# Kernel optimization log

Hardware: AMD Instinct MI355X
Metric: run time of the kernel (lower is better)

Reference implementation:

```python
import jax, jax.numpy as jnp
import numpy as np

FP8_MAX = 448.0  # float8_e4m3fn max
NUM_HEADS = 16

def _fp8_quant_dequant(t):
    # per-(batch, head) symmetric scaling into fp8 e4m3 range, cast to fp8 and back
    amax = jnp.max(jnp.abs(t), axis=(-2, -1), keepdims=True)
    scale = FP8_MAX / jnp.maximum(amax, 1e-12)
    t8 = (t * scale).astype(jnp.float8_e4m3fn).astype(t.dtype)
    return t8 / scale

def setup_inputs() -> dict:
    key = jax.random.key(0)
    k1, k2, k3 = jax.random.split(key, 3)
    B, N, C = 2, 2048, 1024
    x = jax.random.normal(k1, (B, N, C), dtype=jnp.float32)
    w_qkv = jax.random.normal(k2, (C, 3 * C), dtype=jnp.float32) * (C ** -0.5)
    w_proj = jax.random.normal(k3, (C, C), dtype=jnp.float32) * (C ** -0.5)
    b_proj = jnp.zeros((C,), dtype=jnp.float32)
    return {"x": x, "w_qkv": w_qkv, "w_proj": w_proj, "b_proj": b_proj}

def reference(x, w_qkv, w_proj, b_proj):
    B, N, C = x.shape
    H = NUM_HEADS
    D = C // H
    scale = D ** -0.5
    qkv = (x @ w_qkv).reshape(B, N, 3, H, D).transpose(2, 0, 3, 1, 4)  # [3,B,H,N,D]
    q, k, v = qkv[0], qkv[1], qkv[2]
    # sage-style fp8 quantize/dequant of q and k fused into score computation
    q = _fp8_quant_dequant(q)
    k = _fp8_quant_dequant(k)
    scores = jnp.einsum('bhqd,bhkd->bhqk', q, k) * scale  # [B,H,N,N]
    causal = jnp.tril(jnp.ones((N, N), dtype=bool))
    scores = jnp.where(causal[None, None], scores, jnp.finfo(scores.dtype).min)
    attn = jax.nn.softmax(scores, axis=-1)
    out = jnp.einsum('bhqk,bhkd->bhqd', attn, v)  # [B,H,N,D]
    out = out.transpose(0, 2, 1, 3).reshape(B, N, C)
    return out @ w_proj + b_proj
```

## Files before the change

kernel.cpp:

```cpp
#include <hip/hip_runtime.h>

#define B_   2
#define N_   2048
#define C_   1024
#define H_   16
#define D_   64
#define BH_  (B_*H_)
#define NDH  (N_*D_)
#define M1   (B_*N_)

typedef __attribute__((ext_vector_type(4))) float    f32x4;
typedef __attribute__((ext_vector_type(8))) _Float16 f16x8;
typedef __attribute__((ext_vector_type(4))) _Float16 f16x4;
typedef __attribute__((ext_vector_type(2))) __fp16   h16x2;

#define GLOAD_LDS(gp, lp) \
  __builtin_amdgcn_global_load_lds((const __attribute__((address_space(1))) void*)(gp), \
                                   (__attribute__((address_space(3))) void*)(lp), 16, 0, 0)

__global__ __launch_bounds__(256) void k_prep(const float* __restrict__ x,
                                              _Float16* __restrict__ xh,
                                              const float* __restrict__ wq,
                                              const float* __restrict__ wp,
                                              _Float16* __restrict__ whT,
                                              _Float16* __restrict__ wpT,
                                              unsigned* __restrict__ amax_u) {
  __shared__ _Float16 t[64][68];
  int bid = blockIdx.x;
  if (bid < 4096) {
    int i = bid * 256 + threadIdx.x;
    float4 v = ((const float4*)x)[i];
    f16x4 o;
    o.x = (_Float16)v.x; o.y = (_Float16)v.y; o.z = (_Float16)v.z; o.w = (_Float16)v.w;
    ((f16x4*)xh)[i] = o;
    return;
  }
  int idx = bid - 4096;
  if (idx == 0 && threadIdx.x < 64) amax_u[threadIdx.x] = 0u;
  const float* in; _Float16* out; int Cc, cx, cy;
  if (idx < 768) { in = wq; out = whT; Cc = 3072; cx = idx % 48; cy = idx / 48; }
  else { idx -= 768; in = wp; out = wpT; Cc = 1024; cx = idx % 16; cy = idx / 16; }
  const int R = 1024;
  int c0 = cx * 64, r0 = cy * 64;
  int tid = threadIdx.x;
  int cq = tid & 15, rq = tid >> 4;
#pragma unroll
  for (int i = 0; i < 4; ++i) {
    int r = rq + i * 16;
    float4 v = *(const float4*)(in + (size_t)(r0 + r) * Cc + c0 + cq * 4);
    t[r][cq*4+0] = (_Float16)v.x;
    t[r][cq*4+1] = (_Float16)v.y;
    t[r][cq*4+2] = (_Float16)v.z;
    t[r][cq*4+3] = (_Float16)v.w;
  }
  __syncthreads();
#pragma unroll
  for (int i = 0; i < 4; ++i) {
    int c = rq + i * 16;
    f16x4 o;
    o.x = t[cq*4+0][c];
    o.y = t[cq*4+1][c];
    o.z = t[cq*4+2][c];
    o.w = t[cq*4+3][c];
    *(f16x4*)(out + (size_t)(c0 + c) * R + r0 + cq * 4) = o;
  }
}

__global__ __launch_bounds__(256) void k_gemm_qkv(const _Float16* __restrict__ A,
                                                  const _Float16* __restrict__ BT,
                                                  _Float16* __restrict__ qh,
                                                  _Float16* __restrict__ kh,
                                                  _Float16* __restrict__ vh,
                                                  unsigned* __restrict__ amax_u) {
  __shared__ __align__(16) _Float16 As[2][128 * 64];
  __shared__ __align__(16) _Float16 Bs[2][128 * 64];
  const int tid = threadIdx.x, lane = tid & 63, wave = tid >> 6;
  const int wm = wave >> 1, wn = wave & 1;
  const int mcol = lane & 15, quad = lane >> 4;
  const int m0 = blockIdx.x * 128, n0 = blockIdx.y * 128;
  const int swa = mcol & 7;
  f32x4 acc[4][4] = {};

  auto stage = [&](int buf, int k0) {
#pragma unroll
    for (int r = 0; r < 4; ++r) {
      int s = tid + r * 256;
      int row = s >> 3, kc = (s & 7) ^ (row & 7);
      GLOAD_LDS(A  + (size_t)(m0 + row) * 1024 + k0 + kc * 8, &As[buf][s * 8]);
      GLOAD_LDS(BT + (size_t)(n0 + row) * 1024 + k0 + kc * 8, &Bs[buf][s * 8]);
    }
  };
  auto compute = [&](int buf) {
#pragma unroll
    for (int kk = 0; kk < 2; ++kk) {
      f16x8 af[4], bf[4];
#pragma unroll
      for (int tm = 0; tm < 4; ++tm) {
        int row = wm * 64 + tm * 16 + mcol;
        af[tm] = *(const f16x8*)&As[buf][(row * 8 + ((kk * 4 + quad) ^ swa)) * 8];
      }
#pragma unroll
      for (int tn = 0; tn < 4; ++tn) {
        int row = wn * 64 + tn * 16 + mcol;
        bf[tn] = *(const f16x8*)&Bs[buf][(row * 8 + ((kk * 4 + quad) ^ swa)) * 8];
      }
#pragma unroll
      for (int tm = 0; tm < 4; ++tm)
#pragma unroll
        for (int tn = 0; tn < 4; ++tn)
          acc[tm][tn] = __builtin_amdgcn_mfma_f32_16x16x32_f16(af[tm], bf[tn], acc[tm][tn], 0, 0, 0);
    }
  };

  stage(0, 0);
#pragma unroll 1
  for (int t = 0; t < 16; ++t) {
    const int cur = t & 1;
    __builtin_amdgcn_s_barrier();
    if (t + 1 < 16) {
      stage(cur ^ 1, (t + 1) * 64);
      asm volatile("s_waitcnt vmcnt(8)" ::: "memory");
    } else {
      asm volatile("s_waitcnt vmcnt(0)" ::: "memory");
    }
    __builtin_amdgcn_s_barrier();
    __builtin_amdgcn_sched_barrier(0);
    compute(cur);
  }

  const int sec = n0 >> 10;
  if (sec < 2) {
    _Float16* dst = sec ? kh : qh;
    float mxv = 0.f;
#pragma unroll
    for (int tm = 0; tm < 4; ++tm)
#pragma unroll
      for (int tn = 0; tn < 4; ++tn) {
        int rowb = m0 + wm * 64 + tm * 16 + quad * 4;
        int col = n0 + wn * 64 + tn * 16 + mcol;
        int cc = col & 1023, h = cc >> 6, d = cc & 63;
        int b = rowb >> 11, n = rowb & 2047;
        f32x4 a = acc[tm][tn];
        mxv = fmaxf(mxv, fmaxf(fmaxf(fabsf(a[0]), fabsf(a[1])),
                               fmaxf(fabsf(a[2]), fabsf(a[3]))));
        f16x4 o;
        o.x = (_Float16)a[0]; o.y = (_Float16)a[1];
        o.z = (_Float16)a[2]; o.w = (_Float16)a[3];
        *(f16x4*)&dst[(size_t)(b * 16 + h) * 131072 + (size_t)(n >> 5) * 2048 + d * 32 + (n & 31)] = o;
      }
#pragma unroll
    for (int off = 32; off; off >>= 1) mxv = fmaxf(mxv, __shfl_xor(mxv, off));
    if (lane == 0) {
      int head = ((n0 & 1023) >> 6) + wn;
      int plane = (m0 >> 11) * 16 + head;
      atomicMax(&amax_u[sec * 32 + plane], __float_as_uint(mxv));
    }
  } else {
#pragma unroll
    for (int tm = 0; tm < 4; ++tm)
#pragma unroll
      for (int tn = 0; tn < 4; ++tn) {
        int rowb = m0 + wm * 64 + tm * 16 + quad * 4;
        int col = n0 + wn * 64 + tn * 16 + mcol;
        int cc = col & 1023, h = cc >> 6, d = cc & 63;
        int b = rowb >> 11, n = rowb & 2047;
        f16x4 o;
        o.x = (_Float16)acc[tm][tn][0];
        o.y = (_Float16)acc[tm][tn][1];
        o.z = (_Float16)acc[tm][tn][2];
        o.w = (_Float16)acc[tm][tn][3];
        size_t e = (size_t)(b * 16 + h) * 131072 + (size_t)(n >> 5) * 2048
                 + (d >> 4) * 512 + ((n >> 3) & 3) * 128 + (d & 15) * 8 + (n & 7);
        *(f16x4*)&vh[e] = o;
      }
  }
}

__global__ __launch_bounds__(256) void k_quant(const _Float16* __restrict__ qh,
                                               const _Float16* __restrict__ kh,
                                               const float* __restrict__ amax,
                                               char* __restrict__ q8,
                                               char* __restrict__ k8) {
  __shared__ ushort T[32][72];
  int blk = blockIdx.x;
  int which = blk >> 11;
  int idx = blk & 2047;
  int bh = idx >> 6, chunk = idx & 63;
  const _Float16* src = (which ? kh : qh) + (size_t)bh * NDH + chunk * 2048;
  float s = 448.f / fmaxf(amax[which * 32 + bh], 1e-12f);
  int t = threadIdx.x;
  f16x8 v = *(const f16x8*)(src + t * 8);
  int d = t >> 2, kk0 = (t & 3) * 8;
#pragma unroll
  for (int j = 0; j < 8; ++j) T[kk0 + j][d] = ((const ushort*)&v)[j];
  __syncthreads();
  int r = t >> 3, d0 = (t & 7) * 8;
  f16x8 row = *(const f16x8*)&T[r][d0];
  float f[8];
#pragma unroll
  for (int j = 0; j < 8; ++j) f[j] = (float)((const _Float16*)&row)[j] * s;
  int lo = 0, hi = 0;
  lo = __builtin_amdgcn_cvt_pk_fp8_f32(f[0], f[1], lo, false);
  lo = __builtin_amdgcn_cvt_pk_fp8_f32(f[2], f[3], lo, true);
  hi = __builtin_amdgcn_cvt_pk_fp8_f32(f[4], f[5], hi, false);
  hi = __builtin_amdgcn_cvt_pk_fp8_f32(f[6], f[7], hi, true);
  int2 o; o.x = lo; o.y = hi;
  if (which == 0) {
    char* dst = q8 + (size_t)bh * NDH + (size_t)(chunk * 32 + r) * 64 + d0;
    *(int2*)dst = o;
  } else {
    int e = (r >> 2) & 1;
    int mc = (r >> 3) * 4 + (r & 3);
    int kb = d0 >> 5, dq = (d0 >> 3) & 3;
    char* dst = k8 + (size_t)bh * NDH + chunk * 2048 + (e * 2 + kb) * 512 + dq * 128 + mc * 8;
    *(int2*)dst = o;
  }
}

__global__ __launch_bounds__(256) void k_flash(const char* __restrict__ q8,
                                               const char* __restrict__ k8,
                                               const _Float16* __restrict__ vh,
                                               const float* __restrict__ amax,
                                               _Float16* __restrict__ attn) {
  const int bh = blockIdx.x;
  const int tid = threadIdx.x;
  const int wave = tid >> 6, lane = tid & 63;
  const int mcol = lane & 15, quad = lane >> 4;
  const int g = 127 - (blockIdx.y * 4 + wave);
  const int nt = (g >> 3) + 1;
  const int ntmax = ((127 - blockIdx.y * 4) >> 3) + 1;

  __shared__ __align__(16) char     Ks[8192];
  __shared__ __align__(16) _Float16 Vs[8192];

  float sq = 448.f / fmaxf(amax[bh], 1e-12f);
  float sk = 448.f / fmaxf(amax[32 + bh], 1e-12f);
  const float c2 = (1.f / (sq * sk)) * 0.125f * 1.44269504089f;

  const size_t pbase = (size_t)bh * NDH;
  const char* kpl = k8 + pbase;
  const _Float16* vpl = vh + pbase;
  const int qrow = g * 16 + mcol;
  long aq0, aq1;
  { const char* qp = q8 + pbase + (size_t)qrow * 64;
    aq0 = *(const long*)(qp + quad * 8); aq1 = *(const long*)(qp + 32 + quad * 8); }

  f32x4 O[4] = {};
  float m_i = -3e38f, l_i = 0.f;
  const int b = bh >> 4, h = bh & 15;
  const int kq = quad * 8;
  const int koff = quad * 128 + mcol * 8;
  const int voff = quad * 128 + mcol * 8;

#pragma unroll 1
  for (int t = 0; t < ntmax; ++t) {
    {
      const char* ks = kpl + (size_t)t * 8192;
      const _Float16* vs = vpl + (size_t)t * 8192;
#pragma unroll
      for (int r = 0; r < 2; ++r)
        GLOAD_LDS(ks + (tid + r * 256) * 16, &Ks[(tid + r * 256) * 16]);
#pragma unroll
      for (int r = 0; r < 4; ++r)
        GLOAD_LDS(vs + (tid + r * 256) * 8, &Vs[(tid + r * 256) * 8]);
    }
    __syncthreads();

    if (t < nt) {
      const int n0 = t * 128;
      f32x4 s[4][2];
#pragma unroll
      for (int p = 0; p < 4; ++p)
#pragma unroll
        for (int e = 0; e < 2; ++e) {
          long ka = *(const long*)&Ks[(p * 4 + e * 2 + 0) * 512 + koff];
          long kb = *(const long*)&Ks[(p * 4 + e * 2 + 1) * 512 + koff];
          f32x4 z = {};
          z = __builtin_amdgcn_mfma_f32_16x16x32_fp8_fp8(ka, aq0, z, 0, 0, 0);
          z = __builtin_amdgcn_mfma_f32_16x16x32_fp8_fp8(kb, aq1, z, 0, 0, 0);
          s[p][e] = z;
        }
      if (t >= nt - 1) {
#pragma unroll
        for (int p = 0; p < 4; ++p)
#pragma unroll
          for (int e = 0; e < 2; ++e)
#pragma unroll
            for (int r = 0; r < 4; ++r) {
              int key = n0 + p * 32 + kq + e * 4 + r;
              s[p][e][r] = (key <= qrow) ? s[p][e][r] : -3e38f;
            }
      }
      float fm[8];
#pragma unroll
      for (int p = 0; p < 4; ++p)
#pragma unroll
        for (int e = 0; e < 2; ++e) {
          f32x4 v = s[p][e];
          fm[p * 2 + e] = fmaxf(fmaxf(v[0], v[1]), fmaxf(v[2], v[3]));
        }
      float mx = fmaxf(fmaxf(fmaxf(fm[0], fm[1]), fmaxf(fm[2], fm[3])),
                       fmaxf(fmaxf(fm[4], fm[5]), fmaxf(fm[6], fm[7])));
      mx = fmaxf(mx, m_i);
      mx = fmaxf(mx, __shfl_xor(mx, 16));
      mx = fmaxf(mx, __shfl_xor(mx, 32));
      float alpha = __builtin_amdgcn_exp2f((m_i - mx) * c2);
      m_i = mx;
      const float nh = -mx * c2;
      float fs[8];
#pragma unroll
      for (int p = 0; p < 4; ++p)
#pragma unroll
        for (int e = 0; e < 2; ++e) {
          float p0 = __builtin_amdgcn_exp2f(fmaf(s[p][e][0], c2, nh));
          float p1 = __builtin_amdgcn_exp2f(fmaf(s[p][e][1], c2, nh));
          float p2 = __builtin_amdgcn_exp2f(fmaf(s[p][e][2], c2, nh));
          float p3 = __builtin_amdgcn_exp2f(fmaf(s[p][e][3], c2, nh));
          s[p][e][0] = p0; s[p][e][1] = p1; s[p][e][2] = p2; s[p][e][3] = p3;
          fs[p * 2 + e] = (p0 + p1) + (p2 + p3);
        }
      float sum = ((fs[0] + fs[1]) + (fs[2] + fs[3])) + ((fs[4] + fs[5]) + (fs[6] + fs[7]));
      sum += __shfl_xor(sum, 16);
      sum += __shfl_xor(sum, 32);
      l_i = l_i * alpha + sum;
#pragma unroll
      for (int dt = 0; dt < 4; ++dt)
#pragma unroll
        for (int r = 0; r < 4; ++r)
          O[dt][r] *= alpha;
#pragma unroll
      for (int p = 0; p < 4; ++p) {
        f16x8 pb;
        h16x2* pb2 = (h16x2*)&pb;
        pb2[0] = __builtin_amdgcn_cvt_pkrtz(s[p][0][0], s[p][0][1]);
        pb2[1] = __builtin_amdgcn_cvt_pkrtz(s[p][0][2], s[p][0][3]);
        pb2[2] = __builtin_amdgcn_cvt_pkrtz(s[p][1][0], s[p][1][1]);
        pb2[3] = __builtin_amdgcn_cvt_pkrtz(s[p][1][2], s[p][1][3]);
#pragma unroll
        for (int dt = 0; dt < 4; ++dt) {
          f16x8 va = *(const f16x8*)&Vs[p * 2048 + dt * 512 + voff];
          O[dt] = __builtin_amdgcn_mfma_f32_16x16x32_f16(va, pb, O[dt], 0, 0, 0);
        }
      }
    }
    __syncthreads();
  }

  float rl = __builtin_amdgcn_rcpf(l_i);
  _Float16* op = attn + ((size_t)b * 2048 + qrow) * 1024 + h * 64;
#pragma unroll
  for (int dt = 0; dt < 4; ++dt) {
    f16x4 o;
    o.x = (_Float16)(O[dt][0] * rl);
    o.y = (_Float16)(O[dt][1] * rl);
    o.z = (_Float16)(O[dt][2] * rl);
    o.w = (_Float16)(O[dt][3] * rl);
    *(f16x4*)(op + dt * 16 + quad * 4) = o;
  }
}

__global__ __launch_bounds__(256) void k_gemm_out(const _Float16* __restrict__ A,
                                                  const _Float16* __restrict__ BT,
                                                  const float* __restrict__ bias,
                                                  float* __restrict__ out) {
  __shared__ __align__(16) _Float16 As[2][128 * 64];
  __shared__ __align__(16) _Float16 Bs[2][128 * 64];
  const int tid = threadIdx.x, lane = tid & 63, wave = tid >> 6;
  const int wm = wave >> 1, wn = wave & 1;
  const int mcol = lane & 15, quad = lane >> 4;
  const int m0 = blockIdx.x * 128, n0 = blockIdx.y * 128;
  const int swa = mcol & 7;
  f32x4 acc[4][4] = {};

  auto stage = [&](int buf, int k0) {
#pragma unroll
    for (int r = 0; r < 4; ++r) {
      int s = tid + r * 256;
      int row = s >> 3, kc = (s & 7) ^ (row & 7);
      GLOAD_LDS(A  + (size_t)(m0 + row) * 1024 + k0 + kc * 8, &As[buf][s * 8]);
      GLOAD_LDS(BT + (size_t)(n0 + row) * 1024 + k0 + kc * 8, &Bs[buf][s * 8]);
    }
  };
  auto compute = [&](int buf) {
#pragma unroll
    for (int kk = 0; kk < 2; ++kk) {
      f16x8 af[4], bf[4];
#pragma unroll
      for (int tm = 0; tm < 4; ++tm) {
        int row = wm * 64 + tm * 16 + mcol;
        af[tm] = *(const f16x8*)&As[buf][(row * 8 + ((kk * 4 + quad) ^ swa)) * 8];
      }
#pragma unroll
      for (int tn = 0; tn < 4; ++tn) {
        int row = wn * 64 + tn * 16 + mcol;
        bf[tn] = *(const f16x8*)&Bs[buf][(row * 8 + ((kk * 4 + quad) ^ swa)) * 8];
      }
#pragma unroll
      for (int tm = 0; tm < 4; ++tm)
#pragma unroll
        for (int tn = 0; tn < 4; ++tn)
          acc[tm][tn] = __builtin_amdgcn_mfma_f32_16x16x32_f16(af[tm], bf[tn], acc[tm][tn], 0, 0, 0);
    }
  };

  stage(0, 0);
#pragma unroll 1
  for (int t = 0; t < 16; ++t) {
    const int cur = t & 1;
    __builtin_amdgcn_s_barrier();
    if (t + 1 < 16) {
      stage(cur ^ 1, (t + 1) * 64);
      asm volatile("s_waitcnt vmcnt(8)" ::: "memory");
    } else {
      asm volatile("s_waitcnt vmcnt(0)" ::: "memory");
    }
    __builtin_amdgcn_s_barrier();
    __builtin_amdgcn_sched_barrier(0);
    compute(cur);
  }

#pragma unroll
  for (int tm = 0; tm < 4; ++tm)
#pragma unroll
    for (int tn = 0; tn < 4; ++tn)
#pragma unroll
      for (int reg = 0; reg < 4; ++reg) {
        int row = m0 + wm * 64 + tm * 16 + quad * 4 + reg;
        int col = n0 + wn * 64 + tn * 16 + mcol;
        out[(size_t)row * 1024 + col] = acc[tm][tn][reg] + bias[col];
      }
}

extern "C" void kernel_launch(void* const* d_in, const int* in_sizes, int n_in,
                              void* d_out, int out_size, void* d_ws, size_t ws_size,
                              hipStream_t stream) {
  const float* x      = (const float*)d_in[0];
  const float* w_qkv  = (const float*)d_in[1];
  const float* w_proj = (const float*)d_in[2];
  const float* b_proj = (const float*)d_in[3];
  float* out = (float*)d_out;

  char* ws = (char*)d_ws;
  _Float16* xh   = (_Float16*)ws; ws += (size_t)M1 * C_ * 2;
  _Float16* whT  = (_Float16*)ws; ws += (size_t)3 * C_ * C_ * 2;
  _Float16* wpT  = (_Float16*)ws; ws += (size_t)C_ * C_ * 2;
  _Float16* qh   = (_Float16*)ws; ws += (size_t)BH_ * NDH * 2;
  _Float16* kh   = (_Float16*)ws; ws += (size_t)BH_ * NDH * 2;
  _Float16* vh   = (_Float16*)ws; ws += (size_t)BH_ * NDH * 2;
  char*     q8   = (char*)ws;     ws += (size_t)BH_ * NDH;
  char*     k8   = (char*)ws;     ws += (size_t)BH_ * NDH;
  _Float16* attn = (_Float16*)ws; ws += (size_t)M1 * C_ * 2;
  float*    amx  = (float*)ws;    ws += 256;

  k_prep<<<5120, 256, 0, stream>>>(x, xh, w_qkv, w_proj, whT, wpT, (unsigned*)amx);
  k_gemm_qkv<<<dim3(M1 / 128, 3 * C_ / 128), 256, 0, stream>>>(xh, whT, qh, kh, vh, (unsigned*)amx);
  k_quant<<<4096, 256, 0, stream>>>(qh, kh, amx, q8, k8);
  k_flash<<<dim3(32, 32), 256, 0, stream>>>(q8, k8, vh, amx, attn);
  k_gemm_out<<<dim3(M1 / 128, C_ / 128), 256, 0, stream>>>(attn, wpT, b_proj, out);
}
```

Measured before the change: 183.8 us.

## Pair complementary causal query tiles per wave and double-buffer K/V loads

Each wave now handles two 16-row query tiles, one near the end and one near the start of the causal range (pr and 127-pr). This balances work across blocks and lets one K/V tile staged in shared memory feed both tiles, and the grid is halved to match. K/V staging is double-buffered with explicit vmcnt waits so the next tile's global-to-LDS loads overlap compute. The cost is more registers for two accumulator sets and fewer blocks in flight, which may lower occupancy.

```diff
diff --git a/kernel.cpp b/kernel.cpp
--- a/kernel.cpp
+++ b/kernel.cpp
@@ -226,12 +226,13 @@
   const int tid = threadIdx.x;
   const int wave = tid >> 6, lane = tid & 63;
   const int mcol = lane & 15, quad = lane >> 4;
-  const int g = 127 - (blockIdx.y * 4 + wave);
-  const int nt = (g >> 3) + 1;
-  const int ntmax = ((127 - blockIdx.y * 4) >> 3) + 1;
-
-  __shared__ __align__(16) char     Ks[8192];
-  __shared__ __align__(16) _Float16 Vs[8192];
+  const int pr = blockIdx.y * 4 + wave;
+  const int ga = 127 - pr, gb = pr;
+  const int ta  = 16 - (pr >> 3);
+  const int ntb = (pr >> 3) + 1;
+
+  __shared__ __align__(16) char     Ks[2][8192];
+  __shared__ __align__(16) _Float16 Vs[2][8192];
 
   float sq = 448.f / fmaxf(amax[bh], 1e-12f);
   float sk = 448.f / fmaxf(amax[32 + bh], 1e-12f);
@@ -240,122 +241,180 @@
   const size_t pbase = (size_t)bh * NDH;
   const char* kpl = k8 + pbase;
   const _Float16* vpl = vh + pbase;
-  const int qrow = g * 16 + mcol;
-  long aq0, aq1;
-  { const char* qp = q8 + pbase + (size_t)qrow * 64;
-    aq0 = *(const long*)(qp + quad * 8); aq1 = *(const long*)(qp + 32 + quad * 8); }
-
-  f32x4 O[4] = {};
-  float m_i = -3e38f, l_i = 0.f;
+  const int qrowA = ga * 16 + mcol, qrowB = gb * 16 + mcol;
+  long aqA0, aqA1, aqB0, aqB1;
+  { const char* qp = q8 + pbase + (size_t)qrowA * 64;
+    aqA0 = *(const long*)(qp + quad * 8); aqA1 = *(const long*)(qp + 32 + quad * 8); }
+  { const char* qp = q8 + pbase + (size_t)qrowB * 64;
+    aqB0 = *(const long*)(qp + quad * 8); aqB1 = *(const long*)(qp + 32 + quad * 8); }
+
+  f32x4 OA[4] = {}, OB[4] = {};
+  float mA = -3e38f, lA = 0.f, mB = -3e38f, lB = 0.f;
   const int b = bh >> 4, h = bh & 15;
   const int kq = quad * 8;
   const int koff = quad * 128 + mcol * 8;
   const int voff = quad * 128 + mcol * 8;
 
+  auto stage = [&](int buf, int t) {
+    const char* ks = kpl + (size_t)t * 8192;
+    const _Float16* vs = vpl + (size_t)t * 8192;
+#pragma unroll
+    for (int r = 0; r < 2; ++r)
+      GLOAD_LDS(ks + (tid + r * 256) * 16, &Ks[buf][(tid + r * 256) * 16]);
+#pragma unroll
+    for (int r = 0; r < 4; ++r)
+      GLOAD_LDS(vs + (tid + r * 256) * 8, &Vs[buf][(tid + r * 256) * 8]);
+  };
+
+  auto softmax = [&](f32x4 (&s)[4][2], bool last, int qrow, int n0,
+                     float& m_i, float& l_i, f32x4 (&O)[4], f16x8 (&pb)[4]) {
+    if (last) {
+#pragma unroll
+      for (int p = 0; p < 4; ++p)
+#pragma unroll
+        for (int e = 0; e < 2; ++e)
+#pragma unroll
+          for (int r = 0; r < 4; ++r) {
+            int key = n0 + p * 32 + kq + e * 4 + r;
+            s[p][e][r] = (key <= qrow) ? s[p][e][r] : -3e38f;
+          }
+    }
+    float fm[8];
+#pragma unroll
+    for (int p = 0; p < 4; ++p)
+#pragma unroll
+      for (int e = 0; e < 2; ++e) {
+        f32x4 v = s[p][e];
+        fm[p * 2 + e] = fmaxf(fmaxf(v[0], v[1]), fmaxf(v[2], v[3]));
+      }
+    float mx = fmaxf(fmaxf(fmaxf(fm[0], fm[1]), fmaxf(fm[2], fm[3])),
+                     fmaxf(fmaxf(fm[4], fm[5]), fmaxf(fm[6], fm[7])));
+    mx = fmaxf(mx, m_i);
+    mx = fmaxf(mx, __shfl_xor(mx, 16));
+    mx = fmaxf(mx, __shfl_xor(mx, 32));
+    float alpha = __builtin_amdgcn_exp2f((m_i - mx) * c2);
+    m_i = mx;
+    const float nh = -mx * c2;
+    float fs[8];
+#pragma unroll
+    for (int p = 0; p < 4; ++p)
+#pragma unroll
+      for (int e = 0; e < 2; ++e) {
+        float p0 = __builtin_amdgcn_exp2f(fmaf(s[p][e][0], c2, nh));
+        float p1 = __builtin_amdgcn_exp2f(fmaf(s[p][e][1], c2, nh));
+        float p2 = __builtin_amdgcn_exp2f(fmaf(s[p][e][2], c2, nh));
+        float p3 = __builtin_amdgcn_exp2f(fmaf(s[p][e][3], c2, nh));
+        s[p][e][0] = p0; s[p][e][1] = p1; s[p][e][2] = p2; s[p][e][3] = p3;
+        fs[p * 2 + e] = (p0 + p1) + (p2 + p3);
+      }
+    float sum = ((fs[0] + fs[1]) + (fs[2] + fs[3])) + ((fs[4] + fs[5]) + (fs[6] + fs[7]));
+    sum += __shfl_xor(sum, 16);
+    sum += __shfl_xor(sum, 32);
+    l_i = l_i * alpha + sum;
+#pragma unroll
+    for (int dt = 0; dt < 4; ++dt)
+#pragma unroll
+      for (int r = 0; r < 4; ++r)
+        O[dt][r] *= alpha;
+#pragma unroll
+    for (int p = 0; p < 4; ++p) {
+      h16x2* pb2 = (h16x2*)&pb[p];
+      pb2[0] = __builtin_amdgcn_cvt_pkrtz(s[p][0][0], s[p][0][1]);
+      pb2[1] = __builtin_amdgcn_cvt_pkrtz(s[p][0][2], s[p][0][3]);
+      pb2[2] = __builtin_amdgcn_cvt_pkrtz(s[p][1][0], s[p][1][1]);
+      pb2[3] = __builtin_amdgcn_cvt_pkrtz(s[p][1][2], s[p][1][3]);
+    }
+  };
+
+  stage(0, 0);
 #pragma unroll 1
-  for (int t = 0; t < ntmax; ++t) {
-    {
-      const char* ks = kpl + (size_t)t * 8192;
-      const _Float16* vs = vpl + (size_t)t * 8192;
-#pragma unroll
-      for (int r = 0; r < 2; ++r)
-        GLOAD_LDS(ks + (tid + r * 256) * 16, &Ks[(tid + r * 256) * 16]);
-#pragma unroll
-      for (int r = 0; r < 4; ++r)
-        GLOAD_LDS(vs + (tid + r * 256) * 8, &Vs[(tid + r * 256) * 8]);
-    }
-    __syncthreads();
-
-    if (t < nt) {
-      const int n0 = t * 128;
-      f32x4 s[4][2];
-#pragma unroll
-      for (int p = 0; p < 4; ++p)
-#pragma unroll
-        for (int e = 0; e < 2; ++e) {
-          long ka = *(const long*)&Ks[(p * 4 + e * 2 + 0) * 512 + koff];
-          long kb = *(const long*)&Ks[(p * 4 + e * 2 + 1) * 512 + koff];
-          f32x4 z = {};
-          z = __builtin_amdgcn_mfma_f32_16x16x32_fp8_fp8(ka, aq0, z, 0, 0, 0);
-          z = __builtin_amdgcn_mfma_f32_16x16x32_fp8_fp8(kb, aq1, z, 0, 0, 0);
-          s[p][e] = z;
-        }
-      if (t >= nt - 1) {
-#pragma unroll
-        for (int p = 0; p < 4; ++p)
-#pragma unroll
-          for (int e = 0; e < 2; ++e)
-#pragma unroll
-            for (int r = 0; r < 4; ++r) {
-              int key = n0 + p * 32 + kq + e * 4 + r;
-              s[p][e][r] = (key <= qrow) ? s[p][e][r] : -3e38f;
-            }
-      }
-      float fm[8];
-#pragma unroll
-      for (int p = 0; p < 4; ++p)
-#pragma unroll
-        for (int e = 0; e < 2; ++e) {
-          f32x4 v = s[p][e];
-          fm[p * 2 + e] = fmaxf(fmaxf(v[0], v[1]), fmaxf(v[2], v[3]));
-        }
-      float mx = fmaxf(fmaxf(fmaxf(fm[0], fm[1]), fmaxf(fm[2], fm[3])),
-                       fmaxf(fmaxf(fm[4], fm[5]), fmaxf(fm[6], fm[7])));
-      mx = fmaxf(mx, m_i);
-      mx = fmaxf(mx, __shfl_xor(mx, 16));
-      mx = fmaxf(mx, __shfl_xor(mx, 32));
-      float alpha = __builtin_amdgcn_exp2f((m_i - mx) * c2);
-      m_i = mx;
-      const float nh = -mx * c2;
-      float fs[8];
-#pragma unroll
-      for (int p = 0; p < 4; ++p)
-#pragma unroll
-        for (int e = 0; e < 2; ++e) {
-          float p0 = __builtin_amdgcn_exp2f(fmaf(s[p][e][0], c2, nh));
-          float p1 = __builtin_amdgcn_exp2f(fmaf(s[p][e][1], c2, nh));
-          float p2 = __builtin_amdgcn_exp2f(fmaf(s[p][e][2], c2, nh));
-          float p3 = __builtin_amdgcn_exp2f(fmaf(s[p][e][3], c2, nh));
-          s[p][e][0] = p0; s[p][e][1] = p1; s[p][e][2] = p2; s[p][e][3] = p3;
-          fs[p * 2 + e] = (p0 + p1) + (p2 + p3);
-        }
-      float sum = ((fs[0] + fs[1]) + (fs[2] + fs[3])) + ((fs[4] + fs[5]) + (fs[6] + fs[7]));
-      sum += __shfl_xor(sum, 16);
-      sum += __shfl_xor(sum, 32);
-      l_i = l_i * alpha + sum;
-#pragma unroll
-      for (int dt = 0; dt < 4; ++dt)
-#pragma unroll
-        for (int r = 0; r < 4; ++r)
-          O[dt][r] *= alpha;
-#pragma unroll
-      for (int p = 0; p < 4; ++p) {
-        f16x8 pb;
-        h16x2* pb2 = (h16x2*)&pb;
-        pb2[0] = __builtin_amdgcn_cvt_pkrtz(s[p][0][0], s[p][0][1]);
-        pb2[1] = __builtin_amdgcn_cvt_pkrtz(s[p][0][2], s[p][0][3]);
-        pb2[2] = __builtin_amdgcn_cvt_pkrtz(s[p][1][0], s[p][1][1]);
-        pb2[3] = __builtin_amdgcn_cvt_pkrtz(s[p][1][2], s[p][1][3]);
-#pragma unroll
-        for (int dt = 0; dt < 4; ++dt) {
-          f16x8 va = *(const f16x8*)&Vs[p * 2048 + dt * 512 + voff];
-          O[dt] = __builtin_amdgcn_mfma_f32_16x16x32_f16(va, pb, O[dt], 0, 0, 0);
-        }
-      }
-    }
-    __syncthreads();
-  }
-
-  float rl = __builtin_amdgcn_rcpf(l_i);
-  _Float16* op = attn + ((size_t)b * 2048 + qrow) * 1024 + h * 64;
-#pragma unroll
-  for (int dt = 0; dt < 4; ++dt) {
-    f16x4 o;
-    o.x = (_Float16)(O[dt][0] * rl);
-    o.y = (_Float16)(O[dt][1] * rl);
-    o.z = (_Float16)(O[dt][2] * rl);
-    o.w = (_Float16)(O[dt][3] * rl);
-    *(f16x4*)(op + dt * 16 + quad * 4) = o;
+  for (int t = 0; t < ta; ++t) {
+    const int cur = t & 1;
+    __builtin_amdgcn_s_barrier();
+    if (t + 1 < ta) {
+      stage(cur ^ 1, t + 1);
+      asm volatile("s_waitcnt vmcnt(6)" ::: "memory");
+    } else {
+      asm volatile("s_waitcnt vmcnt(0)" ::: "memory");
+    }
+    __builtin_amdgcn_s_barrier();
+    __builtin_amdgcn_sched_barrier(0);
+
+    const bool doB = (t < ntb);
+    const int n0 = t * 128;
+    f32x4 sA[4][2], sB[4][2];
+#pragma unroll
+    for (int p = 0; p < 4; ++p) {
+      long kf0 = *(const long*)&Ks[cur][(p * 4 + 0) * 512 + koff];
+      long kf1 = *(const long*)&Ks[cur][(p * 4 + 1) * 512 + koff];
+      long kf2 = *(const long*)&Ks[cur][(p * 4 + 2) * 512 + koff];
+      long kf3 = *(const long*)&Ks[cur][(p * 4 + 3) * 512 + koff];
+      f32x4 z = {};
+      z = __builtin_amdgcn_mfma_f32_16x16x32_fp8_fp8(kf0, aqA0, z, 0, 0, 0);
+      z = __builtin_amdgcn_mfma_f32_16x16x32_fp8_fp8(kf1, aqA1, z, 0, 0, 0);
+      sA[p][0] = z;
+      z = (f32x4){};
+      z = __builtin_amdgcn_mfma_f32_16x16x32_fp8_fp8(kf2, aqA0, z, 0, 0, 0);
+      z = __builtin_amdgcn_mfma_f32_16x16x32_fp8_fp8(kf3, aqA1, z, 0, 0, 0);
+      sA[p][1] = z;
+      if (doB) {
+        z = (f32x4){};
+        z = __builtin_amdgcn_mfma_f32_16x16x32_fp8_fp8(kf0, aqB0, z, 0, 0, 0);
+        z = __builtin_amdgcn_mfma_f32_16x16x32_fp8_fp8(kf1, aqB1, z, 0, 0, 0);
+        sB[p][0] = z;
+        z = (f32x4){};
+        z = __builtin_amdgcn_mfma_f32_16x16x32_fp8_fp8(kf2, aqB0, z, 0, 0, 0);
+        z = __builtin_amdgcn_mfma_f32_16x16x32_fp8_fp8(kf3, aqB1, z, 0, 0, 0);
+        sB[p][1] = z;
+      }
+    }
+    f16x8 pbA[4], pbB[4];
+    softmax(sA, t == ta - 1, qrowA, n0, mA, lA, OA, pbA);
+    if (doB) softmax(sB, t == ntb - 1, qrowB, n0, mB, lB, OB, pbB);
+#pragma unroll
+    for (int p = 0; p < 4; ++p) {
+      f16x8 va0 = *(const f16x8*)&Vs[cur][p * 2048 + 0 * 512 + voff];
+      f16x8 va1 = *(const f16x8*)&Vs[cur][p * 2048 + 1 * 512 + voff];
+      f16x8 va2 = *(const f16x8*)&Vs[cur][p * 2048 + 2 * 512 + voff];
+      f16x8 va3 = *(const f16x8*)&Vs[cur][p * 2048 + 3 * 512 + voff];
+      OA[0] = __builtin_amdgcn_mfma_f32_16x16x32_f16(va0, pbA[p], OA[0], 0, 0, 0);
+      OA[1] = __builtin_amdgcn_mfma_f32_16x16x32_f16(va1, pbA[p], OA[1], 0, 0, 0);
+      OA[2] = __builtin_amdgcn_mfma_f32_16x16x32_f16(va2, pbA[p], OA[2], 0, 0, 0);
+      OA[3] = __builtin_amdgcn_mfma_f32_16x16x32_f16(va3, pbA[p], OA[3], 0, 0, 0);
+      if (doB) {
+        OB[0] = __builtin_amdgcn_mfma_f32_16x16x32_f16(va0, pbB[p], OB[0], 0, 0, 0);
+        OB[1] = __builtin_amdgcn_mfma_f32_16x16x32_f16(va1, pbB[p], OB[1], 0, 0, 0);
+        OB[2] = __builtin_amdgcn_mfma_f32_16x16x32_f16(va2, pbB[p], OB[2], 0, 0, 0);
+        OB[3] = __builtin_amdgcn_mfma_f32_16x16x32_f16(va3, pbB[p], OB[3], 0, 0, 0);
+      }
+    }
+  }
+
+  {
+    float rl = __builtin_amdgcn_rcpf(lA);
+    _Float16* op = attn + ((size_t)b * 2048 + qrowA) * 1024 + h * 64;
+#pragma unroll
+    for (int dt = 0; dt < 4; ++dt) {
+      f16x4 o;
+      o.x = (_Float16)(OA[dt][0] * rl);
+      o.y = (_Float16)(OA[dt][1] * rl);
+      o.z = (_Float16)(OA[dt][2] * rl);
+      o.w = (_Float16)(OA[dt][3] * rl);
+      *(f16x4*)(op + dt * 16 + quad * 4) = o;
+    }
+  }
+  {
+    float rl = __builtin_amdgcn_rcpf(lB);
+    _Float16* op = attn + ((size_t)b * 2048 + qrowB) * 1024 + h * 64;
+#pragma unroll
+    for (int dt = 0; dt < 4; ++dt) {
+      f16x4 o;
+      o.x = (_Float16)(OB[dt][0] * rl);
+      o.y = (_Float16)(OB[dt][1] * rl);
+      o.z = (_Float16)(OB[dt][2] * rl);
+      o.w = (_Float16)(OB[dt][3] * rl);
+      *(f16x4*)(op + dt * 16 + quad * 4) = o;
+    }
   }
 }
 
@@ -455,6 +514,6 @@
   k_prep<<<5120, 256, 0, stream>>>(x, xh, w_qkv, w_proj, whT, wpT, (unsigned*)amx);
   k_gemm_qkv<<<dim3(M1 / 128, 3 * C_ / 128), 256, 0, stream>>>(xh, whT, qh, kh, vh, (unsigned*)amx);
   k_quant<<<4096, 256, 0, stream>>>(qh, kh, amx, q8, k8);
-  k_flash<<<dim3(32, 32), 256, 0, stream>>>(q8, k8, vh, amx, attn);
+  k_flash<<<dim3(32, 16), 256, 0, stream>>>(q8, k8, vh, amx, attn);
   k_gemm_out<<<dim3(M1 / 128, C_ / 128), 256, 0, stream>>>(attn, wpT, b_proj, out);
 }
```

Measured after the change: 186.5 us. No clear change (+1.4%).
